# Performance work log

Hardware: AMD Instinct MI355X
Metric: run time of the kernel (lower is better)

Reference implementation:

```python
import jax, jax.numpy as jnp
import numpy as np

DIM = 64
HEADS = 8
N = 8  # blocks per spatial dim


def setup_inputs() -> dict:
    key = jax.random.key(0)
    ks = jax.random.split(key, 4)
    B, C, H, W = 8, DIM, 256, 256
    x = jax.random.normal(ks[0], (B, C, H, W), dtype=jnp.float32)
    w_qkv = jax.random.normal(ks[1], (3 * DIM, DIM), dtype=jnp.float32) * 0.05
    w_dw = jax.random.normal(ks[2], (3 * DIM, 1, 3, 3), dtype=jnp.float32) * 0.1
    w_proj = jax.random.normal(ks[3], (DIM, DIM), dtype=jnp.float32) * 0.05
    temperature = jnp.ones((HEADS, 1, 1, 1), dtype=jnp.float32)
    return {"x": x, "w_qkv": w_qkv, "w_dw": w_dw, "w_proj": w_proj,
            "temperature": temperature}


def _block_rearrange(t, B, head, c, h1, w1):
    # b (head c) (h1 N) (w1 N) -> b head c (N N) (h1 w1)
    t = t.reshape(B, head, c, h1, N, w1, N)
    t = t.transpose(0, 1, 2, 4, 6, 3, 5)  # b head c N N h1 w1
    return t.reshape(B, head, c, N * N, h1 * w1)


def reference(x, w_qkv, w_dw, w_proj, temperature):
    B, C, H, W = x.shape
    head = HEADS
    c = C // head
    # H, W chosen divisible by N -> reflect pad is a no-op
    h1, w1 = H // N, W // N

    # 1x1 conv (no bias)
    qkv = jnp.einsum('oc,bchw->bohw', w_qkv, x)
    # 3x3 depthwise conv, padding 1
    qkv = jax.lax.conv_general_dilated(
        qkv, w_dw, window_strides=(1, 1), padding=((1, 1), (1, 1)),
        dimension_numbers=('NCHW', 'OIHW', 'NCHW'),
        feature_group_count=3 * C)
    q, k, v = jnp.split(qkv, 3, axis=1)

    q = _block_rearrange(q, B, head, c, h1, w1)  # [B,head,c,NN,h1*w1]
    k = _block_rearrange(k, B, head, c, h1, w1)
    v = _block_rearrange(v, B, head, c, h1, w1)

    eps = 1e-12
    q = q / jnp.maximum(jnp.linalg.norm(q, axis=-1, keepdims=True), eps)
    k = k / jnp.maximum(jnp.linalg.norm(k, axis=-1, keepdims=True), eps)

    # [B,head,c,NN,NN]
    attn = jnp.einsum('bhcnd,bhcmd->bhcnm', q, k) * temperature[None]
    attn = jax.nn.softmax(attn, axis=-1)
    out = jnp.einsum('bhcnm,bhcmd->bhcnd', attn, v)  # [B,head,c,NN,h1*w1]

    # inverse rearrange: b head c (N N) (h1 w1) -> b (head c) (h1 N) (w1 N)
    out = out.reshape(B, head, c, N, N, h1, w1)
    out = out.transpose(0, 1, 2, 5, 3, 6, 4)  # b head c h1 N w1 N
    out = out.reshape(B, C, H, W)

    out = jnp.einsum('oc,bchw->bohw', w_proj, out)
    return out[:, :, :H, :W]
```

## Files before the change

### kernel.cpp

```cpp
#include <hip/hip_runtime.h>
#include <hip/hip_bf16.h>


typedef __attribute__((ext_vector_type(8))) short short8;
typedef __attribute__((ext_vector_type(4))) float f4;
typedef unsigned short u16;

#define PST 72

__device__ __forceinline__ float tof(u16 u) {
  return __builtin_bit_cast(float, ((unsigned)u) << 16);
}
__device__ __forceinline__ void fsplit(float o, u16& h, u16& l) {
  unsigned u = __builtin_bit_cast(unsigned, o);
  h = (u16)(u >> 16);
  float hf = __builtin_bit_cast(float, u & 0xffff0000u);
  l = (u16)(__builtin_bit_cast(unsigned, o - hf) >> 16);
}
__device__ __forceinline__ short8 ldfrag(const u16* p, int row, int ko) {
  return *(const short8*)&p[row * PST + ko];
}

template <int OC>
__global__ __launch_bounds__(256) void k_pwm(const float* in,
                                             const float* __restrict__ w,
                                             float* outp) {
  constexpr int MT = OC / 64;
  __shared__ u16 XTh[64 * PST], XTl[64 * PST];
  const int t = threadIdx.x;
  const int px = t & 63, cg = t >> 6;
  const int g = (t >> 4) & 3, r16 = t & 15;
  const int oc0 = cg * 16 * MT;
  const size_t pix0 = (size_t)blockIdx.x * 256;
  const int b = (int)(pix0 >> 16);
  const int hwb = (int)(pix0 & 65535);
  const float* ibase = in + ((size_t)b << 22);

  short8 ah[MT][2], al[MT][2];
#pragma unroll
  for (int m = 0; m < MT; ++m)
#pragma unroll
    for (int ks = 0; ks < 2; ++ks) {
      const float* wr = w + (oc0 + m * 16 + r16) * 64 + ks * 32 + g * 8;
      float4 a0 = *(const float4*)wr;
      float4 a1 = *(const float4*)(wr + 4);
      float av[8] = {a0.x, a0.y, a0.z, a0.w, a1.x, a1.y, a1.z, a1.w};
      short8 h8, l8;
#pragma unroll
      for (int e = 0; e < 8; ++e) {
        u16 h, l;
        fsplit(av[e], h, l);
        h8[e] = (short)h;
        l8[e] = (short)l;
      }
      ah[m][ks] = h8;
      al[m][ks] = l8;
    }

  float xr[16];
#pragma unroll
  for (int j = 0; j < 16; ++j)
    xr[j] = ibase[((size_t)(cg * 16 + j) << 16) + hwb + px];

#pragma unroll 1
  for (int tau = 0; tau < 4; ++tau) {
    const int hw0 = hwb + tau * 64;
#pragma unroll
    for (int jh = 0; jh < 2; ++jh) {
      short8 hv, lv;
#pragma unroll
      for (int e = 0; e < 8; ++e) {
        u16 h, l;
        fsplit(xr[jh * 8 + e], h, l);
        hv[e] = (short)h;
        lv[e] = (short)l;
      }
      *(short8*)&XTh[px * PST + cg * 16 + jh * 8] = hv;
      *(short8*)&XTl[px * PST + cg * 16 + jh * 8] = lv;
    }
    __syncthreads();
    if (tau < 3) {
#pragma unroll
      for (int j = 0; j < 16; ++j)
        xr[j] = ibase[((size_t)(cg * 16 + j) << 16) + hw0 + 64 + px];
    }
    float* ob = outp + (((size_t)b * OC) << 16) + hw0;
#pragma unroll
    for (int m = 0; m < MT; ++m)
#pragma unroll
      for (int nt = 0; nt < 4; ++nt) {
        f4 acc;
#pragma unroll
        for (int e = 0; e < 4; ++e) acc[e] = 0.f;
#pragma unroll
        for (int ks = 0; ks < 2; ++ks) {
          short8 bh = ldfrag(XTh, nt * 16 + r16, ks * 32 + g * 8);
          short8 bl = ldfrag(XTl, nt * 16 + r16, ks * 32 + g * 8);
          acc = __builtin_amdgcn_mfma_f32_16x16x32_bf16(ah[m][ks], bh, acc, 0, 0, 0);
          acc = __builtin_amdgcn_mfma_f32_16x16x32_bf16(ah[m][ks], bl, acc, 0, 0, 0);
          acc = __builtin_amdgcn_mfma_f32_16x16x32_bf16(al[m][ks], bh, acc, 0, 0, 0);
        }
#pragma unroll
        for (int e = 0; e < 4; ++e) {
          int oc = oc0 + m * 16 + g * 4 + e;
          ob[((size_t)oc << 16) + nt * 16 + r16] = acc[e];
        }
      }
    __syncthreads();
  }
}

struct ConvData {
  float4 f[2][6];
  float hl[2][6];
  float m[2][3];
};

__device__ __forceinline__ void conv_load(const float* __restrict__ pl, int cd,
                                          int t, ConvData& c) {
#pragma unroll
  for (int rr = 0; rr < 2; ++rr) {
    int r = t + rr * 256;
    int lr = r >> 5, w0 = r & 31;
    int h = cd * 16 + lr;
#pragma unroll
    for (int dy = 0; dy < 3; ++dy) {
      int hy = h + dy - 1;
      c.m[rr][dy] = (hy >= 0 && hy < 256) ? 1.f : 0.f;
      int hyc = hy < 0 ? 0 : (hy > 255 ? 255 : hy);
      const float* rp = pl + hyc * 256;
      c.f[rr][2 * dy] = *(const float4*)(rp + w0 * 8);
      c.f[rr][2 * dy + 1] = *(const float4*)(rp + w0 * 8 + 4);
      c.hl[rr][2 * dy] = rp[w0 ? w0 * 8 - 1 : 0];
      c.hl[rr][2 * dy + 1] = rp[w0 < 31 ? w0 * 8 + 8 : 255];
    }
  }
}

__device__ __forceinline__ void conv_eval8(const float* __restrict__ w9,
                                           const ConvData& c, int rr, int w0,
                                           float o[8]) {
  float wm[9];
#pragma unroll
  for (int dy = 0; dy < 3; ++dy) {
    float mm = c.m[rr][dy];
    wm[3 * dy] = w9[3 * dy] * mm;
    wm[3 * dy + 1] = w9[3 * dy + 1] * mm;
    wm[3 * dy + 2] = w9[3 * dy + 2] * mm;
  }
  float rv[3][10];
#pragma unroll
  for (int dy = 0; dy < 3; ++dy) {
    float4 a = c.f[rr][2 * dy], b4 = c.f[rr][2 * dy + 1];
    rv[dy][0] = w0 ? c.hl[rr][2 * dy] : 0.f;
    rv[dy][1] = a.x;  rv[dy][2] = a.y;  rv[dy][3] = a.z;  rv[dy][4] = a.w;
    rv[dy][5] = b4.x; rv[dy][6] = b4.y; rv[dy][7] = b4.z; rv[dy][8] = b4.w;
    rv[dy][9] = (w0 < 31) ? c.hl[rr][2 * dy + 1] : 0.f;
  }
#pragma unroll
  for (int i = 0; i < 8; ++i) {
    o[i] = fmaf(wm[0], rv[0][i], fmaf(wm[1], rv[0][i + 1], fmaf(wm[2], rv[0][i + 2],
            fmaf(wm[3], rv[1][i], fmaf(wm[4], rv[1][i + 1], fmaf(wm[5], rv[1][i + 2],
            fmaf(wm[6], rv[2][i], fmaf(wm[7], rv[2][i + 1], wm[8] * rv[2][i + 2]))))))));
  }
}

__device__ __forceinline__ void stage_nk(const float* __restrict__ pl,
                                         const float* __restrict__ w9,
                                         u16* __restrict__ ph,
                                         u16* __restrict__ plo, int cd, int t) {
  ConvData c;
  conv_load(pl, cd, t, c);
  const int w0 = t & 31;
#pragma unroll
  for (int rr = 0; rr < 2; ++rr) {
    int lr = (t >> 5) + rr * 8;
    int nb = (lr & 7) * 8;
    int dcol = ((lr >> 3) << 5) + w0;
    float o[8];
    conv_eval8(w9, c, rr, w0, o);
#pragma unroll
    for (int i = 0; i < 8; ++i) {
      u16 h, l;
      fsplit(o[i], h, l);
      ph[(nb + i) * PST + dcol] = h;
      plo[(nb + i) * PST + dcol] = l;
    }
  }
}

__device__ __forceinline__ void stage_vt(const float* __restrict__ pl,
                                         const float* __restrict__ w9,
                                         u16* __restrict__ ph,
                                         u16* __restrict__ plo, int cd, int t) {
  ConvData c;
  conv_load(pl, cd, t, c);
  const int w0 = t & 31;
#pragma unroll
  for (int rr = 0; rr < 2; ++rr) {
    int lr = (t >> 5) + rr * 8;
    int nb = (lr & 7) * 8;
    int dcol = ((lr >> 3) << 5) + w0;
    float o[8];
    conv_eval8(w9, c, rr, w0, o);
    short8 hv, lv;
#pragma unroll
    for (int i = 0; i < 8; ++i) {
      u16 h, l;
      fsplit(o[i], h, l);
      hv[i] = (short)h;
      lv[i] = (short)l;
    }
    *(short8*)&ph[dcol * PST + nb] = hv;
    *(short8*)&plo[dcol * PST + nb] = lv;
  }
}

__global__ __launch_bounds__(256) void k_qkt(float* qkv0,
                                             const float* __restrict__ wdw) {
  __shared__ u16 SAh[64 * PST], SAl[64 * PST];
  __shared__ u16 SBh[64 * PST], SBl[64 * PST];
  __shared__ float red[64 * 8];
  const int t = threadIdx.x;
  const int u = blockIdx.x >> 1, hd = blockIdx.x & 1;
  const int b = u >> 6, ch = u & 63;
  float* qpl = qkv0 + (((size_t)b * 192 + ch) << 16);
  const float* kpl = qkv0 + (((size_t)b * 192 + 64 + ch) << 16);
  float wq[9], wk[9];
#pragma unroll
  for (int i = 0; i < 9; ++i) {
    wq[i] = wdw[ch * 9 + i];
    wk[i] = wdw[(64 + ch) * 9 + i];
  }
  const int wid = t >> 6, g = (t >> 4) & 3, r16 = t & 15;
  f4 acc[4];
#pragma unroll
  for (int cb = 0; cb < 4; ++cb)
#pragma unroll
    for (int e = 0; e < 4; ++e) acc[cb][e] = 0.f;
  float sqQ = 0.f, sqK = 0.f;

  for (int c8 = 0; c8 < 8; ++c8) {
    const int cd = hd * 8 + c8;
    stage_nk(qpl, wq, SAh, SAl, cd, t);
    stage_nk(kpl, wk, SBh, SBl, cd, t);
    __syncthreads();
    {
      const int n = t >> 2, c0 = (t & 3) << 4;
#pragma unroll
      for (int h2 = 0; h2 < 2; ++h2) {
        short8 qh = *(const short8*)&SAh[n * PST + c0 + 8 * h2];
        short8 ql = *(const short8*)&SAl[n * PST + c0 + 8 * h2];
        short8 kh = *(const short8*)&SBh[n * PST + c0 + 8 * h2];
        short8 kl = *(const short8*)&SBl[n * PST + c0 + 8 * h2];
#pragma unroll
        for (int e = 0; e < 8; ++e) {
          float qv = tof((u16)qh[e]) + tof((u16)ql[e]);
          float kv = tof((u16)kh[e]) + tof((u16)kl[e]);
          sqQ = fmaf(qv, qv, sqQ);
          sqK = fmaf(kv, kv, sqK);
        }
      }
    }
#pragma unroll
    for (int ks = 0; ks < 2; ++ks) {
      const int ko = ks * 32 + g * 8;
      short8 ah = ldfrag(SAh, wid * 16 + r16, ko);
      short8 al = ldfrag(SAl, wid * 16 + r16, ko);
#pragma unroll
      for (int cb = 0; cb < 4; ++cb) {
        short8 bh = ldfrag(SBh, cb * 16 + r16, ko);
        short8 bl = ldfrag(SBl, cb * 16 + r16, ko);
        acc[cb] = __builtin_amdgcn_mfma_f32_16x16x32_bf16(ah, bh, acc[cb], 0, 0, 0);
        acc[cb] = __builtin_amdgcn_mfma_f32_16x16x32_bf16(ah, bl, acc[cb], 0, 0, 0);
        acc[cb] = __builtin_amdgcn_mfma_f32_16x16x32_bf16(al, bh, acc[cb], 0, 0, 0);
      }
    }
    __syncthreads();
  }

  red[(t >> 2) * 8 + (t & 3)] = sqQ;
  red[(t >> 2) * 8 + 4 + (t & 3)] = sqK;
  __syncthreads();
  float* stash = qpl + hd * 32768 + 256;
  if (t < 128) {
    int n = t & 63;
    int o = (t >> 6) * 4;
    float s = red[n * 8 + o] + red[n * 8 + o + 1] + red[n * 8 + o + 2] +
              red[n * 8 + o + 3];
    stash[4096 + (t >> 6) * 64 + n] = s;
  }
#pragma unroll
  for (int cb = 0; cb < 4; ++cb)
#pragma unroll
    for (int r = 0; r < 4; ++r) {
      int n = wid * 16 + g * 4 + r, m = cb * 16 + r16;
      stash[n * 64 + m] = acc[cb][r];
    }
}

__global__ __launch_bounds__(256) void k_pv(const float* qkv0,
                                            const float* __restrict__ wdw,
                                            const float* __restrict__ temperature,
                                            float* __restrict__ out) {
  __shared__ u16 Ph[64 * PST], Pl[64 * PST];
  __shared__ u16 Vh[64 * PST], Vl[64 * PST];
  __shared__ float invk[64];
  const int t = threadIdx.x;
  const int u = blockIdx.x >> 1, hd = blockIdx.x & 1;
  const int b = u >> 6, ch = u & 63;
  const float* vpl = qkv0 + (((size_t)b * 192 + 128 + ch) << 16);
  const float* sb0 = qkv0 + (((size_t)b * 192 + ch) << 16) + 256;
  const float* sb1 = sb0 + 32768;
  float wv[9];
#pragma unroll
  for (int i = 0; i < 9; ++i) wv[i] = wdw[(128 + ch) * 9 + i];
  const float tscale = temperature[ch >> 3];
  const int wid = t >> 6, g = (t >> 4) & 3, r16 = t & 15;

  if (t < 64) {
    float s = sb0[4096 + 64 + t] + sb1[4096 + 64 + t];
    invk[t] = 1.f / fmaxf(sqrtf(s), 1e-12f);
  }
  __syncthreads();

  const int row = wid * 16 + r16;
  float sq = sb0[4096 + row] + sb1[4096 + row];
  const float invq = 1.f / fmaxf(sqrtf(sq), 1e-12f);
  float sv[16];
  const float* s0r = sb0 + row * 64 + g * 16;
  const float* s1r = sb1 + row * 64 + g * 16;
  float mx = -1e30f;
#pragma unroll
  for (int j = 0; j < 16; ++j) {
    sv[j] = (s0r[j] + s1r[j]) * invq * invk[g * 16 + j] * tscale;
    mx = fmaxf(mx, sv[j]);
  }
  mx = fmaxf(mx, __shfl_xor(mx, 16));
  mx = fmaxf(mx, __shfl_xor(mx, 32));
  float ss = 0.f;
#pragma unroll
  for (int j = 0; j < 16; ++j) {
    sv[j] = __expf(sv[j] - mx);
    ss += sv[j];
  }
  ss += __shfl_xor(ss, 16);
  ss += __shfl_xor(ss, 32);
  const float rs = 1.f / ss;
  short8 h0, h1, l0, l1;
#pragma unroll
  for (int j = 0; j < 8; ++j) {
    u16 h, l;
    fsplit(sv[j] * rs, h, l);
    h0[j] = (short)h; l0[j] = (short)l;
    fsplit(sv[8 + j] * rs, h, l);
    h1[j] = (short)h; l1[j] = (short)l;
  }
  *(short8*)&Ph[row * PST + g * 16] = h0;
  *(short8*)&Ph[row * PST + g * 16 + 8] = h1;
  *(short8*)&Pl[row * PST + g * 16] = l0;
  *(short8*)&Pl[row * PST + g * 16 + 8] = l1;
  __syncthreads();

  short8 pah[2], pal[2];
#pragma unroll
  for (int ks = 0; ks < 2; ++ks) {
    pah[ks] = ldfrag(Ph, wid * 16 + r16, ks * 32 + g * 8);
    pal[ks] = ldfrag(Pl, wid * 16 + r16, ks * 32 + g * 8);
  }

  size_t obase = ((size_t)b * 64 + ch) << 16;
  for (int c8 = 0; c8 < 8; ++c8) {
    const int cd = hd * 8 + c8;
    stage_vt(vpl, wv, Vh, Vl, cd, t);
    __syncthreads();
    f4 po[4];
#pragma unroll
    for (int cb = 0; cb < 4; ++cb)
#pragma unroll
      for (int e = 0; e < 4; ++e) po[cb][e] = 0.f;
#pragma unroll
    for (int ks = 0; ks < 2; ++ks) {
      const int ko = ks * 32 + g * 8;
#pragma unroll
      for (int cb = 0; cb < 4; ++cb) {
        short8 bh = ldfrag(Vh, cb * 16 + r16, ko);
        short8 bl = ldfrag(Vl, cb * 16 + r16, ko);
        po[cb] = __builtin_amdgcn_mfma_f32_16x16x32_bf16(pah[ks], bh, po[cb], 0, 0, 0);
        po[cb] = __builtin_amdgcn_mfma_f32_16x16x32_bf16(pah[ks], bl, po[cb], 0, 0, 0);
        po[cb] = __builtin_amdgcn_mfma_f32_16x16x32_bf16(pal[ks], bh, po[cb], 0, 0, 0);
      }
    }
#pragma unroll
    for (int cb = 0; cb < 4; ++cb)
#pragma unroll
      for (int r = 0; r < 4; ++r) {
        int n = wid * 16 + g * 4 + r;
        int d = cd * 64 + cb * 16 + r16;
        int hh = ((d >> 5) << 3) + (n >> 3);
        int ww = ((d & 31) << 3) + (n & 7);
        out[obase + hh * 256 + ww] = po[cb][r];
      }
    __syncthreads();
  }
}

extern "C" void kernel_launch(void* const* d_in, const int* in_sizes, int n_in,
                              void* d_out, int out_size, void* d_ws,
                              size_t ws_size, hipStream_t stream) {
  const float* x = (const float*)d_in[0];
  const float* wqkv = (const float*)d_in[1];
  const float* wdw = (const float*)d_in[2];
  const float* wproj = (const float*)d_in[3];
  const float* temp = (const float*)d_in[4];
  float* out = (float*)d_out;
  float* qkv0 = (float*)d_ws;

  k_pwm<192><<<2048, 256, 0, stream>>>(x, wqkv, qkv0);
  k_qkt<<<1024, 256, 0, stream>>>(qkv0, wdw);
  k_pv<<<1024, 256, 0, stream>>>(qkv0, wdw, temp, out);
  k_pwm<64><<<2048, 256, 0, stream>>>(out, wproj, out);
}
```

Before: 363.3 us.

## Prefetch depthwise-conv input rows into LDS via async global_load_lds

The per-thread register loads of the 3x3 halo rows are replaced with async global-to-LDS loads of 18 raw rows per chunk, issued for the next chunk right after staging the current one. The conv then reads its inputs from LDS, so the global load latency overlaps the MFMA work and the redundant halo reads across threads are removed. This adds 36KB or 18KB of LDS per block, which can reduce occupancy. It also relies on waitcnt plus barrier ordering, and one trailing barrier per iteration is dropped.

```diff
diff --git a/kernel.cpp b/kernel.cpp
--- a/kernel.cpp
+++ b/kernel.cpp
@@ -19,6 +19,12 @@
 }
 __device__ __forceinline__ short8 ldfrag(const u16* p, int row, int ko) {
   return *(const short8*)&p[row * PST + ko];
+}
+
+__device__ __forceinline__ void gload_row(const float* g, float* l) {
+  __builtin_amdgcn_global_load_lds(
+      (const __attribute__((address_space(1))) unsigned*)g,
+      (__attribute__((address_space(3))) unsigned*)l, 16, 0, 0);
 }
 
 template <int OC>
@@ -110,52 +116,27 @@
   }
 }
 
-struct ConvData {
-  float4 f[2][6];
-  float hl[2][6];
-  float m[2][3];
-};
-
-__device__ __forceinline__ void conv_load(const float* __restrict__ pl, int cd,
-                                          int t, ConvData& c) {
-#pragma unroll
-  for (int rr = 0; rr < 2; ++rr) {
-    int r = t + rr * 256;
-    int lr = r >> 5, w0 = r & 31;
-    int h = cd * 16 + lr;
-#pragma unroll
-    for (int dy = 0; dy < 3; ++dy) {
-      int hy = h + dy - 1;
-      c.m[rr][dy] = (hy >= 0 && hy < 256) ? 1.f : 0.f;
-      int hyc = hy < 0 ? 0 : (hy > 255 ? 255 : hy);
-      const float* rp = pl + hyc * 256;
-      c.f[rr][2 * dy] = *(const float4*)(rp + w0 * 8);
-      c.f[rr][2 * dy + 1] = *(const float4*)(rp + w0 * 8 + 4);
-      c.hl[rr][2 * dy] = rp[w0 ? w0 * 8 - 1 : 0];
-      c.hl[rr][2 * dy + 1] = rp[w0 < 31 ? w0 * 8 + 8 : 255];
-    }
-  }
-}
-
-__device__ __forceinline__ void conv_eval8(const float* __restrict__ w9,
-                                           const ConvData& c, int rr, int w0,
-                                           float o[8]) {
-  float wm[9];
+__device__ __forceinline__ void conv_eval_lds(const float* __restrict__ raw,
+                                              const float* __restrict__ w9,
+                                              int lr, int w0, int cd,
+                                              float o[8]) {
+  float wm[9], rv[3][10];
 #pragma unroll
   for (int dy = 0; dy < 3; ++dy) {
-    float mm = c.m[rr][dy];
+    int hy = cd * 16 + lr - 1 + dy;
+    float mm = (hy >= 0 && hy < 256) ? 1.f : 0.f;
     wm[3 * dy] = w9[3 * dy] * mm;
     wm[3 * dy + 1] = w9[3 * dy + 1] * mm;
     wm[3 * dy + 2] = w9[3 * dy + 2] * mm;
-  }
-  float rv[3][10];
-#pragma unroll
-  for (int dy = 0; dy < 3; ++dy) {
-    float4 a = c.f[rr][2 * dy], b4 = c.f[rr][2 * dy + 1];
-    rv[dy][0] = w0 ? c.hl[rr][2 * dy] : 0.f;
-    rv[dy][1] = a.x;  rv[dy][2] = a.y;  rv[dy][3] = a.z;  rv[dy][4] = a.w;
-    rv[dy][5] = b4.x; rv[dy][6] = b4.y; rv[dy][7] = b4.z; rv[dy][8] = b4.w;
-    rv[dy][9] = (w0 < 31) ? c.hl[rr][2 * dy + 1] : 0.f;
+    const float* rp = raw + (lr + dy) * 256;
+    float4 l0 = *(const float4*)(rp + w0 * 8);
+    float4 l1 = *(const float4*)(rp + w0 * 8 + 4);
+    float sL = rp[w0 ? w0 * 8 - 1 : 0];
+    float sR = rp[w0 * 8 + 8];
+    rv[dy][0] = w0 ? sL : 0.f;
+    rv[dy][1] = l0.x; rv[dy][2] = l0.y; rv[dy][3] = l0.z; rv[dy][4] = l0.w;
+    rv[dy][5] = l1.x; rv[dy][6] = l1.y; rv[dy][7] = l1.z; rv[dy][8] = l1.w;
+    rv[dy][9] = (w0 < 31) ? sR : 0.f;
   }
 #pragma unroll
   for (int i = 0; i < 8; ++i) {
@@ -165,59 +146,37 @@
   }
 }
 
-__device__ __forceinline__ void stage_nk(const float* __restrict__ pl,
-                                         const float* __restrict__ w9,
-                                         u16* __restrict__ ph,
-                                         u16* __restrict__ plo, int cd, int t) {
-  ConvData c;
-  conv_load(pl, cd, t, c);
-  const int w0 = t & 31;
-#pragma unroll
-  for (int rr = 0; rr < 2; ++rr) {
-    int lr = (t >> 5) + rr * 8;
-    int nb = (lr & 7) * 8;
-    int dcol = ((lr >> 3) << 5) + w0;
-    float o[8];
-    conv_eval8(w9, c, rr, w0, o);
-#pragma unroll
-    for (int i = 0; i < 8; ++i) {
-      u16 h, l;
-      fsplit(o[i], h, l);
-      ph[(nb + i) * PST + dcol] = h;
-      plo[(nb + i) * PST + dcol] = l;
-    }
-  }
-}
-
-__device__ __forceinline__ void stage_vt(const float* __restrict__ pl,
-                                         const float* __restrict__ w9,
-                                         u16* __restrict__ ph,
-                                         u16* __restrict__ plo, int cd, int t) {
-  ConvData c;
-  conv_load(pl, cd, t, c);
-  const int w0 = t & 31;
-#pragma unroll
-  for (int rr = 0; rr < 2; ++rr) {
-    int lr = (t >> 5) + rr * 8;
-    int nb = (lr & 7) * 8;
-    int dcol = ((lr >> 3) << 5) + w0;
-    float o[8];
-    conv_eval8(w9, c, rr, w0, o);
-    short8 hv, lv;
-#pragma unroll
-    for (int i = 0; i < 8; ++i) {
-      u16 h, l;
-      fsplit(o[i], h, l);
-      hv[i] = (short)h;
-      lv[i] = (short)l;
-    }
-    *(short8*)&ph[dcol * PST + nb] = hv;
-    *(short8*)&plo[dcol * PST + nb] = lv;
+__device__ __forceinline__ void issue_raw_qk(const float* qpl, const float* kpl,
+                                             float* rawQ, float* rawK, int cd,
+                                             int wid, int lane) {
+  const float* src = (wid & 2) ? kpl : qpl;
+  float* dst = (wid & 2) ? rawK : rawQ;
+#pragma unroll
+  for (int j = 0; j < 9; ++j) {
+    int rr = (wid & 1) * 9 + j;
+    int hy = cd * 16 - 1 + rr;
+    hy = hy < 0 ? 0 : (hy > 255 ? 255 : hy);
+    gload_row(src + hy * 256 + lane * 4, dst + rr * 256);
+  }
+}
+
+__device__ __forceinline__ void issue_raw_v(const float* vpl, float* rawV,
+                                            int cd, int wid, int lane) {
+#pragma unroll
+  for (int j = 0; j < 5; ++j) {
+    int rr = wid * 5 + j;
+    if (rr < 18) {
+      int hy = cd * 16 - 1 + rr;
+      hy = hy < 0 ? 0 : (hy > 255 ? 255 : hy);
+      gload_row(vpl + hy * 256 + lane * 4, rawV + rr * 256);
+    }
   }
 }
 
 __global__ __launch_bounds__(256) void k_qkt(float* qkv0,
                                              const float* __restrict__ wdw) {
+  __shared__ float rawQ[18 * 256];
+  __shared__ float rawK[18 * 256];
   __shared__ u16 SAh[64 * PST], SAl[64 * PST];
   __shared__ u16 SBh[64 * PST], SBl[64 * PST];
   __shared__ float red[64 * 8];
@@ -226,13 +185,18 @@
   const int b = u >> 6, ch = u & 63;
   float* qpl = qkv0 + (((size_t)b * 192 + ch) << 16);
   const float* kpl = qkv0 + (((size_t)b * 192 + 64 + ch) << 16);
+  const int wid = t >> 6, lane = t & 63;
+  const int g = (t >> 4) & 3, r16 = t & 15;
+  const int lr0 = t >> 5, w0 = t & 31;
+
+  issue_raw_qk(qpl, kpl, rawQ, rawK, hd * 8, wid, lane);
+
   float wq[9], wk[9];
 #pragma unroll
   for (int i = 0; i < 9; ++i) {
     wq[i] = wdw[ch * 9 + i];
     wk[i] = wdw[(64 + ch) * 9 + i];
   }
-  const int wid = t >> 6, g = (t >> 4) & 3, r16 = t & 15;
   f4 acc[4];
 #pragma unroll
   for (int cb = 0; cb < 4; ++cb)
@@ -240,11 +204,33 @@
     for (int e = 0; e < 4; ++e) acc[cb][e] = 0.f;
   float sqQ = 0.f, sqK = 0.f;
 
+#pragma unroll 1
   for (int c8 = 0; c8 < 8; ++c8) {
     const int cd = hd * 8 + c8;
-    stage_nk(qpl, wq, SAh, SAl, cd, t);
-    stage_nk(kpl, wk, SBh, SBl, cd, t);
-    __syncthreads();
+    asm volatile("s_waitcnt vmcnt(0)" ::: "memory");
+    __syncthreads();
+#pragma unroll
+    for (int rr = 0; rr < 2; ++rr) {
+      int lr = lr0 + rr * 8;
+      int nb = (lr & 7) * 8;
+      int dcol = ((lr >> 3) << 5) + w0;
+      float oq[8], ok[8];
+      conv_eval_lds(rawQ, wq, lr, w0, cd, oq);
+      conv_eval_lds(rawK, wk, lr, w0, cd, ok);
+#pragma unroll
+      for (int i = 0; i < 8; ++i) {
+        u16 h, l;
+        fsplit(oq[i], h, l);
+        SAh[(nb + i) * PST + dcol] = h;
+        SAl[(nb + i) * PST + dcol] = l;
+        fsplit(ok[i], h, l);
+        SBh[(nb + i) * PST + dcol] = h;
+        SBl[(nb + i) * PST + dcol] = l;
+      }
+    }
+    __syncthreads();
+    if (c8 < 7)
+      issue_raw_qk(qpl, kpl, rawQ, rawK, cd + 1, wid, lane);
     {
       const int n = t >> 2, c0 = (t & 3) << 4;
 #pragma unroll
@@ -276,9 +262,9 @@
         acc[cb] = __builtin_amdgcn_mfma_f32_16x16x32_bf16(al, bh, acc[cb], 0, 0, 0);
       }
     }
-    __syncthreads();
-  }
-
+  }
+
+  __syncthreads();
   red[(t >> 2) * 8 + (t & 3)] = sqQ;
   red[(t >> 2) * 8 + 4 + (t & 3)] = sqK;
   __syncthreads();
@@ -303,6 +289,7 @@
                                             const float* __restrict__ wdw,
                                             const float* __restrict__ temperature,
                                             float* __restrict__ out) {
+  __shared__ float rawV[18 * 256];
   __shared__ u16 Ph[64 * PST], Pl[64 * PST];
   __shared__ u16 Vh[64 * PST], Vl[64 * PST];
   __shared__ float invk[64];
@@ -312,11 +299,16 @@
   const float* vpl = qkv0 + (((size_t)b * 192 + 128 + ch) << 16);
   const float* sb0 = qkv0 + (((size_t)b * 192 + ch) << 16) + 256;
   const float* sb1 = sb0 + 32768;
+  const int wid = t >> 6, lane = t & 63;
+  const int g = (t >> 4) & 3, r16 = t & 15;
+  const int lr0 = t >> 5, w0 = t & 31;
+
+  issue_raw_v(vpl, rawV, hd * 8, wid, lane);
+
   float wv[9];
 #pragma unroll
   for (int i = 0; i < 9; ++i) wv[i] = wdw[(128 + ch) * 9 + i];
   const float tscale = temperature[ch >> 3];
-  const int wid = t >> 6, g = (t >> 4) & 3, r16 = t & 15;
 
   if (t < 64) {
     float s = sb0[4096 + 64 + t] + sb1[4096 + 64 + t];
@@ -370,10 +362,31 @@
   }
 
   size_t obase = ((size_t)b * 64 + ch) << 16;
+#pragma unroll 1
   for (int c8 = 0; c8 < 8; ++c8) {
     const int cd = hd * 8 + c8;
-    stage_vt(vpl, wv, Vh, Vl, cd, t);
-    __syncthreads();
+    asm volatile("s_waitcnt vmcnt(0)" ::: "memory");
+    __syncthreads();
+#pragma unroll
+    for (int rr = 0; rr < 2; ++rr) {
+      int lr = lr0 + rr * 8;
+      int nb = (lr & 7) * 8;
+      int dcol = ((lr >> 3) << 5) + w0;
+      float o[8];
+      conv_eval_lds(rawV, wv, lr, w0, cd, o);
+      short8 hv, lv;
+#pragma unroll
+      for (int i = 0; i < 8; ++i) {
+        u16 h, l;
+        fsplit(o[i], h, l);
+        hv[i] = (short)h;
+        lv[i] = (short)l;
+      }
+      *(short8*)&Vh[dcol * PST + nb] = hv;
+      *(short8*)&Vl[dcol * PST + nb] = lv;
+    }
+    __syncthreads();
+    if (c8 < 7) issue_raw_v(vpl, rawV, cd + 1, wid, lane);
     f4 po[4];
 #pragma unroll
     for (int cb = 0; cb < 4; ++cb)
@@ -401,7 +414,6 @@
         int ww = ((d & 31) << 3) + (n & 7);
         out[obase + hh * 256 + ww] = po[cb][r];
       }
-    __syncthreads();
   }
 }
 
```

Result: faster. 313.6 us (-13.7%).
